# Performance work log

Hardware: AMD Instinct MI355X
Metric: run time of the kernel (lower is better)

The kernel has to match this reference:

```python
import jax, jax.numpy as jnp
import numpy as np

C = 19
IGNORE = 255
UPPER_BOUND = 1.0
SEG_W, EDGE_W, ATT_W = 1.0, 0.3, 0.1
EDGE_THRESH = 0.8


def _img_hist(t):
    # torch.histc(target, bins=C, min=0, max=C): bin i counts values in [i, i+1); 255 falls outside
    tf = t.ravel()
    inb = (tf >= 0) & (tf < C)
    idx = jnp.where(inb, tf, 0)
    return jnp.zeros((C,), jnp.float32).at[idx].add(inb.astype(jnp.float32))


def _seg_loss(segin, target):
    # per-image class-histogram weights (ImageBasedCrossEntropyLoss2d, norm=False)
    N = target.shape[0]
    bins = jax.vmap(_img_hist)(target)                      # [N, C]
    hist_norm = bins / jnp.sum(bins, axis=1, keepdims=True)
    w = (bins != 0).astype(jnp.float32) * UPPER_BOUND * (1.0 - hist_norm) + 1.0  # [N, C]

    logp = jax.nn.log_softmax(segin, axis=1)                # [N, C, H, W]
    tc = jnp.clip(target, 0, C - 1)
    lp = jnp.take_along_axis(logp, tc[:, None, :, :], axis=1)[:, 0]  # [N, H, W]
    valid = (target != IGNORE).astype(jnp.float32)
    pw = jnp.take_along_axis(w, tc.reshape(N, -1), axis=1).reshape(target.shape) * valid
    # NLLLoss(weight, reduction='mean', ignore_index): weighted mean per image, summed over batch
    num = -jnp.sum(pw * lp, axis=(1, 2))
    den = jnp.sum(pw, axis=(1, 2))
    return jnp.sum(num / den)


def _bce2d(x, t):
    # x: logits [N,1,H,W]; t: float target, 1=pos, 0=neg, >1 ignored (weight 0)
    pos = t == 1.0
    neg = t == 0.0
    pos_num = jnp.sum(pos.astype(jnp.float32))
    neg_num = jnp.sum(neg.astype(jnp.float32))
    sum_num = pos_num + neg_num
    w = jnp.where(pos, neg_num / sum_num, 0.0) + jnp.where(neg, pos_num / sum_num, 0.0)
    # stable BCE-with-logits
    bce = jnp.maximum(x, 0.0) - x * t + jnp.log1p(jnp.exp(-jnp.abs(x)))
    return jnp.mean(w * bce)


def setup_inputs() -> dict:
    key = jax.random.key(0)
    k1, k2, k3, k4 = jax.random.split(key, 4)
    N, H, W = 4, 768, 768
    segin = jax.random.normal(k1, (N, C, H, W), dtype=jnp.float32)
    edgein = jax.random.normal(k2, (N, 1, H, W), dtype=jnp.float32)
    segmask = jax.random.randint(k3, (N, H, W), 0, C, dtype=jnp.int32)
    edgemask = jax.random.randint(k4, (N, 1, H, W), 0, 2, dtype=jnp.int32)
    return {"segin": segin, "edgein": edgein, "segmask": segmask, "edgemask": edgemask}


def reference(segin, edgein, segmask, edgemask):
    seg_loss = SEG_W * _seg_loss(segin, segmask)
    edge_loss = EDGE_W * _bce2d(edgein, edgemask.astype(jnp.float32))
    # edge attention: pixels where max-channel edge logit > 0.8 keep their label, else ignore
    edge_max = jnp.max(edgein, axis=1)                      # [N, H, W]
    att_target = jnp.where(edge_max > EDGE_THRESH, segmask, IGNORE)
    att_loss = ATT_W * _seg_loss(segin, att_target)
    return seg_loss + edge_loss + att_loss
```

## Files before the change

### kernel.cpp

```cpp
#include <hip/hip_runtime.h>
#include <math.h>

#define CNUM 19
#define NB 4
#define HW 589824
#define NPIX 2359296

#define TPB 256
#define PXT 8
#define TILE (TPB * PXT)
#define G1 1024

struct ImgAcc2 {
  double sS[CNUM];
  double sA[CNUM];
  unsigned int cS[CNUM];
  unsigned int cA[CNUM];
  unsigned int pad[2];
};

struct Ws {
  ImgAcc2 img[NB];
  double bce_p, bce_n;
  unsigned int np, nn;
};

__global__ void k_init(Ws* ws) {
  unsigned int* p = (unsigned int*)ws;
  const int nw = (int)(sizeof(Ws) / 4);
  for (int i = threadIdx.x; i < nw; i += blockDim.x) p[i] = 0u;
}

__global__ __launch_bounds__(TPB) void k_fused(const float* __restrict__ segin,
                                               const float* __restrict__ edgein,
                                               const int* __restrict__ segmask,
                                               const int* __restrict__ edgemask,
                                               Ws* __restrict__ wsw) {
  const int n = blockIdx.y;
  const int t = threadIdx.x;
  const int tile0 = blockIdx.x * TILE;

  __shared__ float lsS[4][CNUM + 1], lsA[4][CNUM + 1];
  __shared__ unsigned int lcS[4][CNUM + 1], lcA[4][CNUM + 1];
  __shared__ float sbp, sbn;
  __shared__ unsigned int snp, snn;

  if (t < 4 * (CNUM + 1)) {
    ((float*)lsS)[t] = 0.f; ((float*)lsA)[t] = 0.f;
    ((unsigned int*)lcS)[t] = 0u; ((unsigned int*)lcA)[t] = 0u;
  }
  if (t == 128) { sbp = 0.f; sbn = 0.f; snp = 0u; snn = 0u; }
  __syncthreads();

  const int px0 = n * HW + tile0 + t * 4;
  const int px1 = px0 + G1;

  int4 tm0 = *reinterpret_cast<const int4*>(segmask + px0);
  int4 tm1 = *reinterpret_cast<const int4*>(segmask + px1);
  int tcv[PXT];
  unsigned int inbits = 0u;
  {
    int ta[PXT] = {tm0.x, tm0.y, tm0.z, tm0.w, tm1.x, tm1.y, tm1.z, tm1.w};
    #pragma unroll
    for (int j = 0; j < PXT; ++j) {
      tcv[j] = min(max(ta[j], 0), CNUM - 1);
      inbits |= (((unsigned)ta[j]) < (unsigned)CNUM) ? (1u << j) : 0u;
    }
  }

  float sacc[PXT], xt[PXT];
  #pragma unroll
  for (int j = 0; j < PXT; ++j) { sacc[j] = 0.f; xt[j] = 0.f; }

  const float* cb = segin + (size_t)n * CNUM * HW + tile0 + t * 4;
  #pragma unroll
  for (int c = 0; c < CNUM; ++c) {
    const float* p = cb + (size_t)c * HW;
    float4 v0 = *reinterpret_cast<const float4*>(p);
    float4 v1 = *reinterpret_cast<const float4*>(p + G1);
    float va[PXT] = {v0.x, v0.y, v0.z, v0.w, v1.x, v1.y, v1.z, v1.w};
    #pragma unroll
    for (int j = 0; j < PXT; ++j) {
      sacc[j] += __expf(va[j]);
      xt[j] = (tcv[j] == c) ? va[j] : xt[j];
    }
  }

  float4 e0 = *reinterpret_cast<const float4*>(edgein + px0);
  float4 e1 = *reinterpret_cast<const float4*>(edgein + px1);
  int4   m0 = *reinterpret_cast<const int4*>(edgemask + px0);
  int4   m1 = *reinterpret_cast<const int4*>(edgemask + px1);

  const int wv = t >> 6;
  float bpos = 0.f, bneg = 0.f;
  int cntp = 0, cntn = 0;
  {
    float ea[PXT] = {e0.x, e0.y, e0.z, e0.w, e1.x, e1.y, e1.z, e1.w};
    int   ma[PXT] = {m0.x, m0.y, m0.z, m0.w, m1.x, m1.y, m1.z, m1.w};
    #pragma unroll
    for (int j = 0; j < PXT; ++j) {
      float nlp = __logf(sacc[j]) - xt[j];
      if ((inbits >> j) & 1u) {
        atomicAdd(&lsS[wv][tcv[j]], nlp);
        atomicAdd(&lcS[wv][tcv[j]], 1u);
        if (ea[j] > 0.8f) {
          atomicAdd(&lsA[wv][tcv[j]], nlp);
          atomicAdd(&lcA[wv][tcv[j]], 1u);
        }
      }
      float e = ea[j];
      int m = ma[j];
      float bce = fmaxf(e, 0.f) - e * (float)m + log1pf(__expf(-fabsf(e)));
      if (m == 1) { bpos += bce; ++cntp; }
      else if (m == 0) { bneg += bce; ++cntn; }
    }
  }

  #pragma unroll
  for (int off = 32; off > 0; off >>= 1) {
    bpos += __shfl_down(bpos, off);
    bneg += __shfl_down(bneg, off);
    cntp += __shfl_down(cntp, off);
    cntn += __shfl_down(cntn, off);
  }
  if ((t & 63) == 0) {
    atomicAdd(&sbp, bpos);
    atomicAdd(&sbn, bneg);
    atomicAdd(&snp, (unsigned int)cntp);
    atomicAdd(&snn, (unsigned int)cntn);
  }
  __syncthreads();

  if (t < CNUM) {
    float v = lsS[0][t] + lsS[1][t] + lsS[2][t] + lsS[3][t];
    atomicAdd(&wsw->img[n].sS[t], (double)v);
  } else if (t >= 32 && t < 32 + CNUM) {
    int c = t - 32;
    float v = lsA[0][c] + lsA[1][c] + lsA[2][c] + lsA[3][c];
    atomicAdd(&wsw->img[n].sA[c], (double)v);
  } else if (t >= 64 && t < 64 + CNUM) {
    int c = t - 64;
    unsigned int v = lcS[0][c] + lcS[1][c] + lcS[2][c] + lcS[3][c];
    if (v) atomicAdd(&wsw->img[n].cS[c], v);
  } else if (t >= 96 && t < 96 + CNUM) {
    int c = t - 96;
    unsigned int v = lcA[0][c] + lcA[1][c] + lcA[2][c] + lcA[3][c];
    if (v) atomicAdd(&wsw->img[n].cA[c], v);
  } else if (t == 128) {
    atomicAdd(&wsw->bce_p, (double)sbp);
  } else if (t == 129) {
    atomicAdd(&wsw->bce_n, (double)sbn);
  } else if (t == 130) {
    atomicAdd(&wsw->np, snp);
  } else if (t == 131) {
    atomicAdd(&wsw->nn, snn);
  }
}

__global__ void k_final(const Ws* __restrict__ ws, float* __restrict__ out) {
  if (threadIdx.x == 0 && blockIdx.x == 0) {
    double segl = 0.0, attl = 0.0;
    for (int i = 0; i < NB; ++i) {
      const ImgAcc2* a = &ws->img[i];
      double totS = 0.0, totA = 0.0;
      for (int c = 0; c < CNUM; ++c) { totS += (double)a->cS[c]; totA += (double)a->cA[c]; }
      double numS = 0.0, denS = 0.0, numA = 0.0, denA = 0.0;
      for (int c = 0; c < CNUM; ++c) {
        double bS = (double)a->cS[c];
        double wS = (bS != 0.0 ? (1.0 - bS / totS) : 0.0) + 1.0;
        numS += wS * a->sS[c];
        denS += wS * bS;
        double bA = (double)a->cA[c];
        double wA = (bA != 0.0 ? (1.0 - bA / totA) : 0.0) + 1.0;
        numA += wA * a->sA[c];
        denA += wA * bA;
      }
      segl += numS / denS;
      attl += numA / denA;
    }
    double s = (double)ws->np + (double)ws->nn;
    double wpos = (double)ws->nn / s;
    double wneg = (double)ws->np / s;
    double edgel = (wpos * ws->bce_p + wneg * ws->bce_n) / (double)NPIX;
    out[0] = (float)(segl + 0.3 * edgel + 0.1 * attl);
  }
}

extern "C" void kernel_launch(void* const* d_in, const int* in_sizes, int n_in,
                              void* d_out, int out_size, void* d_ws, size_t ws_size,
                              hipStream_t stream) {
  const float* segin   = (const float*)d_in[0];
  const float* edgein  = (const float*)d_in[1];
  const int*   segmask = (const int*)d_in[2];
  const int*   edgemask= (const int*)d_in[3];
  Ws* ws = (Ws*)d_ws;
  float* out = (float*)d_out;

  hipLaunchKernelGGL(k_init,  dim3(1),             dim3(256), 0, stream, ws);
  hipLaunchKernelGGL(k_fused, dim3(HW / TILE, NB), dim3(TPB), 0, stream, segin, edgein, segmask, edgemask, ws);
  hipLaunchKernelGGL(k_final, dim3(1),             dim3(1),   0, stream, ws, out);
}
```

Baseline: 301.6 us.

## Stream segin channels through per-wave LDS ring via async global_load_lds

Replaces the direct register loads of all 19 channels with an 8-deep per-wave LDS ring buffer filled by global_load_lds (direct global-to-LDS DMA). Manual vmcnt waits and sched barriers pipeline the channel loads. Each thread now handles 4 pixels instead of 8, and blocks grow to 512 threads. The aim is to keep more memory requests in flight with lower register pressure, at the cost of 64KB of LDS per block, which limits occupancy, and fragile hand-placed waitcnt handling.

```diff
diff --git a/kernel.cpp b/kernel.cpp
--- a/kernel.cpp
+++ b/kernel.cpp
@@ -1,15 +1,20 @@
 #include <hip/hip_runtime.h>
 #include <math.h>
+#include <stdint.h>
 
 #define CNUM 19
 #define NB 4
 #define HW 589824
 #define NPIX 2359296
 
-#define TPB 256
-#define PXT 8
-#define TILE (TPB * PXT)
-#define G1 1024
+#define TPB 512
+#define WAVES 8
+#define WPX 256
+#define TILE (WAVES * WPX)
+#define DEPTH 8
+
+typedef __attribute__((address_space(3))) void lds_void;
+typedef const __attribute__((address_space(1))) void glb_void;
 
 struct ImgAcc2 {
   double sS[CNUM];
@@ -39,81 +44,101 @@
   const int n = blockIdx.y;
   const int t = threadIdx.x;
   const int tile0 = blockIdx.x * TILE;
-
-  __shared__ float lsS[4][CNUM + 1], lsA[4][CNUM + 1];
-  __shared__ unsigned int lcS[4][CNUM + 1], lcA[4][CNUM + 1];
+  const int wv = t >> 6;
+  const int lane = t & 63;
+
+  __shared__ float ring[WAVES][DEPTH][256];
+  __shared__ float lsS[WAVES][CNUM + 1], lsA[WAVES][CNUM + 1];
+  __shared__ unsigned int lcS[WAVES][CNUM + 1], lcA[WAVES][CNUM + 1];
   __shared__ float sbp, sbn;
   __shared__ unsigned int snp, snn;
 
-  if (t < 4 * (CNUM + 1)) {
+  if (t < WAVES * (CNUM + 1)) {
     ((float*)lsS)[t] = 0.f; ((float*)lsA)[t] = 0.f;
     ((unsigned int*)lcS)[t] = 0u; ((unsigned int*)lcA)[t] = 0u;
   }
-  if (t == 128) { sbp = 0.f; sbn = 0.f; snp = 0u; snn = 0u; }
+  if (t == WAVES * (CNUM + 1)) { sbp = 0.f; sbn = 0.f; snp = 0u; snn = 0u; }
   __syncthreads();
 
-  const int px0 = n * HW + tile0 + t * 4;
-  const int px1 = px0 + G1;
-
-  int4 tm0 = *reinterpret_cast<const int4*>(segmask + px0);
-  int4 tm1 = *reinterpret_cast<const int4*>(segmask + px1);
-  int tcv[PXT];
+  const int pxg = n * HW + tile0 + wv * WPX + lane * 4;
+
+  int4   tm = *reinterpret_cast<const int4*>(segmask + pxg);
+  float4 ev = *reinterpret_cast<const float4*>(edgein + pxg);
+  int4   em = *reinterpret_cast<const int4*>(edgemask + pxg);
+
+  int tcv[4];
   unsigned int inbits = 0u;
+  float ea[4] = {ev.x, ev.y, ev.z, ev.w};
+  int   ma[4] = {em.x, em.y, em.z, em.w};
   {
-    int ta[PXT] = {tm0.x, tm0.y, tm0.z, tm0.w, tm1.x, tm1.y, tm1.z, tm1.w};
-    #pragma unroll
-    for (int j = 0; j < PXT; ++j) {
+    int ta[4] = {tm.x, tm.y, tm.z, tm.w};
+    #pragma unroll
+    for (int j = 0; j < 4; ++j) {
       tcv[j] = min(max(ta[j], 0), CNUM - 1);
       inbits |= (((unsigned)ta[j]) < (unsigned)CNUM) ? (1u << j) : 0u;
     }
   }
 
-  float sacc[PXT], xt[PXT];
-  #pragma unroll
-  for (int j = 0; j < PXT; ++j) { sacc[j] = 0.f; xt[j] = 0.f; }
-
-  const float* cb = segin + (size_t)n * CNUM * HW + tile0 + t * 4;
-  #pragma unroll
-  for (int c = 0; c < CNUM; ++c) {
-    const float* p = cb + (size_t)c * HW;
-    float4 v0 = *reinterpret_cast<const float4*>(p);
-    float4 v1 = *reinterpret_cast<const float4*>(p + G1);
-    float va[PXT] = {v0.x, v0.y, v0.z, v0.w, v1.x, v1.y, v1.z, v1.w};
-    #pragma unroll
-    for (int j = 0; j < PXT; ++j) {
-      sacc[j] += __expf(va[j]);
-      xt[j] = (tcv[j] == c) ? va[j] : xt[j];
-    }
-  }
-
-  float4 e0 = *reinterpret_cast<const float4*>(edgein + px0);
-  float4 e1 = *reinterpret_cast<const float4*>(edgein + px1);
-  int4   m0 = *reinterpret_cast<const int4*>(edgemask + px0);
-  int4   m1 = *reinterpret_cast<const int4*>(edgemask + px1);
-
-  const int wv = t >> 6;
+  asm volatile("s_waitcnt vmcnt(0)" ::: "memory");
+  __builtin_amdgcn_sched_barrier(0);
+
+  const float* srcc = segin + (size_t)n * CNUM * HW + tile0 + wv * WPX + lane * 4;
+
+#define STAGE(c, s)                                                         \
+  __builtin_amdgcn_global_load_lds(                                         \
+      (glb_void*)(srcc + (size_t)(c) * HW),                                 \
+      (lds_void*)(&ring[wv][(s)][0]), 16, 0, 0)
+
+  STAGE(0, 0); STAGE(1, 1); STAGE(2, 2); STAGE(3, 3);
+  STAGE(4, 4); STAGE(5, 5); STAGE(6, 6);
+
+  float sacc[4] = {0.f, 0.f, 0.f, 0.f};
+  float xt[4]   = {0.f, 0.f, 0.f, 0.f};
+
+#define STEP(c, K)                                                          \
+  do {                                                                      \
+    __builtin_amdgcn_sched_barrier(0);                                      \
+    if ((c) + DEPTH - 1 < CNUM)                                             \
+      STAGE((c) + DEPTH - 1, ((c) + DEPTH - 1) & (DEPTH - 1));              \
+    asm volatile("s_waitcnt vmcnt(" #K ")" ::: "memory");                   \
+    __builtin_amdgcn_sched_barrier(0);                                      \
+    {                                                                       \
+      float4 v4 = *reinterpret_cast<const float4*>(                         \
+          &ring[wv][(c) & (DEPTH - 1)][lane * 4]);                          \
+      sacc[0] += __expf(v4.x); xt[0] = (tcv[0] == (c)) ? v4.x : xt[0];      \
+      sacc[1] += __expf(v4.y); xt[1] = (tcv[1] == (c)) ? v4.y : xt[1];      \
+      sacc[2] += __expf(v4.z); xt[2] = (tcv[2] == (c)) ? v4.z : xt[2];      \
+      sacc[3] += __expf(v4.w); xt[3] = (tcv[3] == (c)) ? v4.w : xt[3];      \
+    }                                                                       \
+  } while (0)
+
+  STEP(0, 7);  STEP(1, 7);  STEP(2, 7);  STEP(3, 7);
+  STEP(4, 7);  STEP(5, 7);  STEP(6, 7);  STEP(7, 7);
+  STEP(8, 7);  STEP(9, 7);  STEP(10, 7); STEP(11, 7);
+  STEP(12, 6); STEP(13, 5); STEP(14, 4); STEP(15, 3);
+  STEP(16, 2); STEP(17, 1); STEP(18, 0);
+
+#undef STEP
+#undef STAGE
+
   float bpos = 0.f, bneg = 0.f;
   int cntp = 0, cntn = 0;
-  {
-    float ea[PXT] = {e0.x, e0.y, e0.z, e0.w, e1.x, e1.y, e1.z, e1.w};
-    int   ma[PXT] = {m0.x, m0.y, m0.z, m0.w, m1.x, m1.y, m1.z, m1.w};
-    #pragma unroll
-    for (int j = 0; j < PXT; ++j) {
-      float nlp = __logf(sacc[j]) - xt[j];
-      if ((inbits >> j) & 1u) {
-        atomicAdd(&lsS[wv][tcv[j]], nlp);
-        atomicAdd(&lcS[wv][tcv[j]], 1u);
-        if (ea[j] > 0.8f) {
-          atomicAdd(&lsA[wv][tcv[j]], nlp);
-          atomicAdd(&lcA[wv][tcv[j]], 1u);
-        }
+  #pragma unroll
+  for (int j = 0; j < 4; ++j) {
+    float nlp = __logf(sacc[j]) - xt[j];
+    if ((inbits >> j) & 1u) {
+      atomicAdd(&lsS[wv][tcv[j]], nlp);
+      atomicAdd(&lcS[wv][tcv[j]], 1u);
+      if (ea[j] > 0.8f) {
+        atomicAdd(&lsA[wv][tcv[j]], nlp);
+        atomicAdd(&lcA[wv][tcv[j]], 1u);
       }
-      float e = ea[j];
-      int m = ma[j];
-      float bce = fmaxf(e, 0.f) - e * (float)m + log1pf(__expf(-fabsf(e)));
-      if (m == 1) { bpos += bce; ++cntp; }
-      else if (m == 0) { bneg += bce; ++cntn; }
     }
+    float e = ea[j];
+    int m = ma[j];
+    float bce = fmaxf(e, 0.f) - e * (float)m + log1pf(__expf(-fabsf(e)));
+    if (m == 1) { bpos += bce; ++cntp; }
+    else if (m == 0) { bneg += bce; ++cntn; }
   }
 
   #pragma unroll
@@ -123,7 +148,7 @@
     cntp += __shfl_down(cntp, off);
     cntn += __shfl_down(cntn, off);
   }
-  if ((t & 63) == 0) {
+  if (lane == 0) {
     atomicAdd(&sbp, bpos);
     atomicAdd(&sbn, bneg);
     atomicAdd(&snp, (unsigned int)cntp);
@@ -132,19 +157,27 @@
   __syncthreads();
 
   if (t < CNUM) {
-    float v = lsS[0][t] + lsS[1][t] + lsS[2][t] + lsS[3][t];
+    float v = 0.f;
+    #pragma unroll
+    for (int w = 0; w < WAVES; ++w) v += lsS[w][t];
     atomicAdd(&wsw->img[n].sS[t], (double)v);
   } else if (t >= 32 && t < 32 + CNUM) {
     int c = t - 32;
-    float v = lsA[0][c] + lsA[1][c] + lsA[2][c] + lsA[3][c];
+    float v = 0.f;
+    #pragma unroll
+    for (int w = 0; w < WAVES; ++w) v += lsA[w][c];
     atomicAdd(&wsw->img[n].sA[c], (double)v);
   } else if (t >= 64 && t < 64 + CNUM) {
     int c = t - 64;
-    unsigned int v = lcS[0][c] + lcS[1][c] + lcS[2][c] + lcS[3][c];
+    unsigned int v = 0u;
+    #pragma unroll
+    for (int w = 0; w < WAVES; ++w) v += lcS[w][c];
     if (v) atomicAdd(&wsw->img[n].cS[c], v);
   } else if (t >= 96 && t < 96 + CNUM) {
     int c = t - 96;
-    unsigned int v = lcA[0][c] + lcA[1][c] + lcA[2][c] + lcA[3][c];
+    unsigned int v = 0u;
+    #pragma unroll
+    for (int w = 0; w < WAVES; ++w) v += lcA[w][c];
     if (v) atomicAdd(&wsw->img[n].cA[c], v);
   } else if (t == 128) {
     atomicAdd(&wsw->bce_p, (double)sbp);
```

After: 306.6 us. Within noise of the previous version (+1.7%).

## Split channel loop across waves and combine partial softmax sums in LDS

Applied to the files above, without the earlier changes.

Each wave now handles a strided subset of the 19 channels for the whole 2048-pixel tile, rather than each thread looping over all channels for its own 8 pixels. Per-wave partial exp sums are combined with LDS atomics, and the target logit is written to LDS by the wave that owns that channel. A software prefetch double-buffers the next channel's loads. The aim is more independent memory requests in flight per thread, at the cost of extra LDS traffic, LDS atomics and a second pass that reloads segmask, edgein and edgemask.

```diff
diff --git a/kernel.cpp b/kernel.cpp
--- a/kernel.cpp
+++ b/kernel.cpp
@@ -1,5 +1,6 @@
 #include <hip/hip_runtime.h>
 #include <math.h>
+#include <stdint.h>
 
 #define CNUM 19
 #define NB 4
@@ -7,9 +8,8 @@
 #define NPIX 2359296
 
 #define TPB 256
-#define PXT 8
-#define TILE (TPB * PXT)
-#define G1 1024
+#define TILE 2048
+#define GRP 8
 
 struct ImgAcc2 {
   double sS[CNUM];
@@ -38,82 +38,123 @@
                                                Ws* __restrict__ wsw) {
   const int n = blockIdx.y;
   const int t = threadIdx.x;
+  const int wv = t >> 6;
+  const int lane = t & 63;
   const int tile0 = blockIdx.x * TILE;
 
+  __shared__ float sacc_l[TILE];
+  __shared__ float xt_l[TILE];
   __shared__ float lsS[4][CNUM + 1], lsA[4][CNUM + 1];
   __shared__ unsigned int lcS[4][CNUM + 1], lcA[4][CNUM + 1];
   __shared__ float sbp, sbn;
   __shared__ unsigned int snp, snn;
 
+  for (int i = t; i < TILE; i += TPB) sacc_l[i] = 0.f;
   if (t < 4 * (CNUM + 1)) {
     ((float*)lsS)[t] = 0.f; ((float*)lsA)[t] = 0.f;
     ((unsigned int*)lcS)[t] = 0u; ((unsigned int*)lcA)[t] = 0u;
   }
-  if (t == 128) { sbp = 0.f; sbn = 0.f; snp = 0u; snn = 0u; }
+  if (t == 4 * (CNUM + 1)) { sbp = 0.f; sbn = 0.f; snp = 0u; snn = 0u; }
   __syncthreads();
 
-  const int px0 = n * HW + tile0 + t * 4;
-  const int px1 = px0 + G1;
-
-  int4 tm0 = *reinterpret_cast<const int4*>(segmask + px0);
-  int4 tm1 = *reinterpret_cast<const int4*>(segmask + px1);
-  int tcv[PXT];
-  unsigned int inbits = 0u;
-  {
-    int ta[PXT] = {tm0.x, tm0.y, tm0.z, tm0.w, tm1.x, tm1.y, tm1.z, tm1.w};
+  const int pxbase = n * HW + tile0 + lane * 4;
+  unsigned int tcp[GRP];
+  #pragma unroll
+  for (int g = 0; g < GRP; ++g) {
+    int4 tm = *reinterpret_cast<const int4*>(segmask + pxbase + g * 256);
+    int a0 = min(max(tm.x, 0), CNUM - 1);
+    int a1 = min(max(tm.y, 0), CNUM - 1);
+    int a2 = min(max(tm.z, 0), CNUM - 1);
+    int a3 = min(max(tm.w, 0), CNUM - 1);
+    tcp[g] = (unsigned)a0 | ((unsigned)a1 << 8) | ((unsigned)a2 << 16) | ((unsigned)a3 << 24);
+  }
+
+  float sa[GRP][4], xv[GRP][4];
+  #pragma unroll
+  for (int g = 0; g < GRP; ++g) {
     #pragma unroll
-    for (int j = 0; j < PXT; ++j) {
-      tcv[j] = min(max(ta[j], 0), CNUM - 1);
-      inbits |= (((unsigned)ta[j]) < (unsigned)CNUM) ? (1u << j) : 0u;
-    }
-  }
-
-  float sacc[PXT], xt[PXT];
-  #pragma unroll
-  for (int j = 0; j < PXT; ++j) { sacc[j] = 0.f; xt[j] = 0.f; }
-
-  const float* cb = segin + (size_t)n * CNUM * HW + tile0 + t * 4;
-  #pragma unroll
-  for (int c = 0; c < CNUM; ++c) {
-    const float* p = cb + (size_t)c * HW;
-    float4 v0 = *reinterpret_cast<const float4*>(p);
-    float4 v1 = *reinterpret_cast<const float4*>(p + G1);
-    float va[PXT] = {v0.x, v0.y, v0.z, v0.w, v1.x, v1.y, v1.z, v1.w};
+    for (int j = 0; j < 4; ++j) { sa[g][j] = 0.f; xv[g][j] = 0.f; }
+  }
+
+  const float* sb = segin + (size_t)n * CNUM * HW + tile0 + lane * 4;
+
+  float4 buf[GRP];
+  #pragma unroll
+  for (int g = 0; g < GRP; ++g)
+    buf[g] = *reinterpret_cast<const float4*>(sb + (size_t)wv * HW + g * 256);
+
+  #pragma unroll
+  for (int cc = 0; cc < 5; ++cc) {
+    const int c = wv + cc * 4;
+    if (c < CNUM) {
+      float4 cur[GRP];
+      #pragma unroll
+      for (int g = 0; g < GRP; ++g) cur[g] = buf[g];
+      const int cn = c + 4;
+      if (cn < CNUM) {
+        #pragma unroll
+        for (int g = 0; g < GRP; ++g)
+          buf[g] = *reinterpret_cast<const float4*>(sb + (size_t)cn * HW + g * 256);
+      }
+      #pragma unroll
+      for (int g = 0; g < GRP; ++g) {
+        float va[4] = {cur[g].x, cur[g].y, cur[g].z, cur[g].w};
+        #pragma unroll
+        for (int j = 0; j < 4; ++j) {
+          sa[g][j] += __expf(va[j]);
+          int tcj = (int)((tcp[g] >> (8 * j)) & 255u);
+          xv[g][j] = (tcj == c) ? va[j] : xv[g][j];
+        }
+      }
+    }
+  }
+
+  #pragma unroll
+  for (int g = 0; g < GRP; ++g) {
+    const int px = g * 256 + lane * 4;
     #pragma unroll
-    for (int j = 0; j < PXT; ++j) {
-      sacc[j] += __expf(va[j]);
-      xt[j] = (tcv[j] == c) ? va[j] : xt[j];
-    }
-  }
-
-  float4 e0 = *reinterpret_cast<const float4*>(edgein + px0);
-  float4 e1 = *reinterpret_cast<const float4*>(edgein + px1);
-  int4   m0 = *reinterpret_cast<const int4*>(edgemask + px0);
-  int4   m1 = *reinterpret_cast<const int4*>(edgemask + px1);
-
-  const int wv = t >> 6;
+    for (int j = 0; j < 4; ++j) {
+      atomicAdd(&sacc_l[px + j], sa[g][j]);
+      int tcj = (int)((tcp[g] >> (8 * j)) & 255u);
+      if ((tcj & 3) == wv) xt_l[px + j] = xv[g][j];
+    }
+  }
+  __syncthreads();
+
+  const int ep = t * 8;
+  const int gpx = n * HW + tile0 + ep;
+  int4   sm0 = *reinterpret_cast<const int4*>(segmask + gpx);
+  int4   sm1 = *reinterpret_cast<const int4*>(segmask + gpx + 4);
+  float4 ev0 = *reinterpret_cast<const float4*>(edgein + gpx);
+  float4 ev1 = *reinterpret_cast<const float4*>(edgein + gpx + 4);
+  int4   em0 = *reinterpret_cast<const int4*>(edgemask + gpx);
+  int4   em1 = *reinterpret_cast<const int4*>(edgemask + gpx + 4);
+
+  int   smv[8] = {sm0.x, sm0.y, sm0.z, sm0.w, sm1.x, sm1.y, sm1.z, sm1.w};
+  float eav[8] = {ev0.x, ev0.y, ev0.z, ev0.w, ev1.x, ev1.y, ev1.z, ev1.w};
+  int   emv[8] = {em0.x, em0.y, em0.z, em0.w, em1.x, em1.y, em1.z, em1.w};
+
   float bpos = 0.f, bneg = 0.f;
   int cntp = 0, cntn = 0;
-  {
-    float ea[PXT] = {e0.x, e0.y, e0.z, e0.w, e1.x, e1.y, e1.z, e1.w};
-    int   ma[PXT] = {m0.x, m0.y, m0.z, m0.w, m1.x, m1.y, m1.z, m1.w};
-    #pragma unroll
-    for (int j = 0; j < PXT; ++j) {
-      float nlp = __logf(sacc[j]) - xt[j];
-      if ((inbits >> j) & 1u) {
-        atomicAdd(&lsS[wv][tcv[j]], nlp);
-        atomicAdd(&lcS[wv][tcv[j]], 1u);
-        if (ea[j] > 0.8f) {
-          atomicAdd(&lsA[wv][tcv[j]], nlp);
-          atomicAdd(&lcA[wv][tcv[j]], 1u);
-        }
-      }
-      float e = ea[j];
-      int m = ma[j];
-      float bce = fmaxf(e, 0.f) - e * (float)m + log1pf(__expf(-fabsf(e)));
-      if (m == 1) { bpos += bce; ++cntp; }
-      else if (m == 0) { bneg += bce; ++cntn; }
-    }
+  #pragma unroll
+  for (int k = 0; k < 8; ++k) {
+    float nlp = __logf(sacc_l[ep + k]) - xt_l[ep + k];
+    int tgt = smv[k];
+    int tcc = min(max(tgt, 0), CNUM - 1);
+    bool valid = ((unsigned)tgt) < (unsigned)CNUM;
+    if (valid) {
+      atomicAdd(&lsS[wv][tcc], nlp);
+      atomicAdd(&lcS[wv][tcc], 1u);
+      if (eav[k] > 0.8f) {
+        atomicAdd(&lsA[wv][tcc], nlp);
+        atomicAdd(&lcA[wv][tcc], 1u);
+      }
+    }
+    float e = eav[k];
+    int m = emv[k];
+    float bce = fmaxf(e, 0.f) - e * (float)m + log1pf(__expf(-fabsf(e)));
+    if (m == 1) { bpos += bce; ++cntp; }
+    else if (m == 0) { bneg += bce; ++cntn; }
   }
 
   #pragma unroll
@@ -123,7 +164,7 @@
     cntp += __shfl_down(cntp, off);
     cntn += __shfl_down(cntn, off);
   }
-  if ((t & 63) == 0) {
+  if (lane == 0) {
     atomicAdd(&sbp, bpos);
     atomicAdd(&sbn, bneg);
     atomicAdd(&snp, (unsigned int)cntp);
```

Result: slower. 355.5 us (+17.9%).
